# Kernel optimization log

Hardware: AMD Instinct MI355X
Metric: run time of the kernel (lower is better)

## Reference

```python
import jax, jax.numpy as jnp
import numpy as np

B, S, IK, IV = 16, 2048, 3, 1
D = IK + IV          # input_size = 4
H = 256              # hidden_size
F = 512              # dim_feedforward
L = 2                # num_layers
EPS = 1e-5


def setup_inputs() -> dict:
    key = jax.random.key(0)
    ks = jax.random.split(key, 16)
    n = jax.random.normal
    inp = {
        'KEY': n(ks[0], (B, S, IK), jnp.float32),
        'VALUE': n(ks[1], (B, S, IV), jnp.float32),
        # per-layer kernel-attention projections (stacked on layer axis)
        'Wq': n(ks[2], (L, D, H), jnp.float32) * 0.1,
        'bq': jnp.zeros((L, H), jnp.float32),
        'Wk': n(ks[3], (L, D, H), jnp.float32) * 0.1,
        'bk': jnp.zeros((L, H), jnp.float32),
        'Wv': n(ks[4], (L, D, H), jnp.float32) * 0.1,
        'bv': jnp.zeros((L, H), jnp.float32),
        'Wo': n(ks[5], (L, H, D), jnp.float32) * 0.1,
        'bo': jnp.zeros((L, D), jnp.float32),
        'bw': jnp.ones((L,), jnp.float32),          # Gaussian kernel bandwidth
        # LayerNorm 1
        'g1': jnp.ones((L, D), jnp.float32),
        'be1': jnp.zeros((L, D), jnp.float32),
        # FFN
        'W1': n(ks[6], (L, D, F), jnp.float32) * 0.1,
        'b1': jnp.zeros((L, F), jnp.float32),
        'W2': n(ks[7], (L, F, D), jnp.float32) * 0.1,
        'b2': jnp.zeros((L, D), jnp.float32),
        # LayerNorm 2
        'g2': jnp.ones((L, D), jnp.float32),
        'be2': jnp.zeros((L, D), jnp.float32),
        # final fc: input_size -> input_v
        'Wfc': n(ks[8], (D, IV), jnp.float32) * 0.1,
        'bfc': jnp.zeros((IV,), jnp.float32),
    }
    return inp


def _layernorm(x, g, b):
    m = x.mean(-1, keepdims=True)
    v = ((x - m) ** 2).mean(-1, keepdims=True)
    return (x - m) * jax.lax.rsqrt(v + EPS) * g + b


def reference(KEY, VALUE, Wq, bq, Wk, bk, Wv, bv, Wo, bo, bw,
              g1, be1, W1, b1, W2, b2, g2, be2, Wfc, bfc):
    # positioning: concat coords and values -> [B, S, D]
    X = jnp.concatenate([KEY, VALUE], axis=-1)
    n_layers = Wq.shape[0]
    for i in range(n_layers):
        # Nadaraya-Watson Gaussian kernel attention (madsnn, type='nwd', kernel='gauss')
        Q = X @ Wq[i] + bq[i]                      # [B,S,H]
        K = X @ Wk[i] + bk[i]                      # [B,S,H]
        V = X @ Wv[i] + bv[i]                      # [B,S,H]
        # pairwise squared distances ||q-k||^2, [B,S,S]
        d2 = ((Q * Q).sum(-1)[:, :, None]
              + (K * K).sum(-1)[:, None, :]
              - 2.0 * jnp.einsum('bqh,bkh->bqk', Q, K))
        attn = jax.nn.softmax(-0.5 * d2 * (bw[i] ** 2), axis=-1)
        attn_out = jnp.einsum('bqk,bkh->bqh', attn, V) @ Wo[i] + bo[i]  # [B,S,D]
        # residual + LayerNorm + FFN + residual + LayerNorm (dropout = identity in eval)
        res = _layernorm(X + attn_out, g1[i], be1[i])
        ff = jax.nn.relu(res @ W1[i] + b1[i]) @ W2[i] + b2[i]
        X = _layernorm(res + ff, g2[i], be2[i])
    return X @ Wfc + bfc                            # [B,S,IV]
```

## Files before the change

kernel.cpp:

```cpp
#include <hip/hip_runtime.h>

#define BB 16
#define SS 2048
#define NTOK (BB*SS)
#define FF 512
#define EPSF 1e-5f

#if __has_builtin(__builtin_amdgcn_exp2f)
#define EXP2F(x) __builtin_amdgcn_exp2f(x)
#else
#define EXP2F(x) exp2f(x)
#endif

typedef float v2f __attribute__((ext_vector_type(2)));


__device__ __forceinline__ float wred64(float v) {
#pragma unroll
  for (int m = 32; m > 0; m >>= 1) v += __shfl_xor(v, m, 64);
  return v;
}


__global__ __launch_bounds__(64) void prep_kernel(
    const float* __restrict__ Wq, const float* __restrict__ bq,
    const float* __restrict__ Wk, const float* __restrict__ bk,
    const float* __restrict__ Wv, const float* __restrict__ bv,
    const float* __restrict__ Wo, const float* __restrict__ bw,
    const float* __restrict__ W1, const float* __restrict__ b1,
    const float* __restrict__ W2,
    float* __restrict__ sm, float* __restrict__ w1t)
{
  const int i = blockIdx.x;
  const int lane = threadIdx.x;
  float m4[4][4] = {{0}}, gkk[4][4] = {{0}}, wvo[4][4] = {{0}};
  float akk[4] = {0}, bvo[4] = {0};
  float ck1 = 0.f, ck2 = 0.f;

  for (int h = lane; h < 256; h += 64) {
    float vq[4], vk[4], vv[4], wo4[4];
#pragma unroll
    for (int a = 0; a < 4; ++a) {
      vq[a]  = Wq[(i*4 + a)*256 + h];
      vk[a]  = Wk[(i*4 + a)*256 + h];
      vv[a]  = Wv[(i*4 + a)*256 + h];
      wo4[a] = Wo[(i*256 + h)*4 + a];
    }
    const float bqh = bq[i*256 + h], bkh = bk[i*256 + h], bvh = bv[i*256 + h];
#pragma unroll
    for (int a = 0; a < 4; ++a) {
#pragma unroll
      for (int c = 0; c < 4; ++c) {
        m4[a][c]  = fmaf(vq[a], vk[c], m4[a][c]);
        gkk[a][c] = fmaf(vk[a], vk[c], gkk[a][c]);
        wvo[a][c] = fmaf(vv[a], wo4[c], wvo[a][c]);
      }
      akk[a] = fmaf(vk[a], bqh - bkh, akk[a]);
      bvo[a] = fmaf(bvh, wo4[a], bvo[a]);
    }
    ck1 = fmaf(bqh, bkh, ck1);
    ck2 = fmaf(bkh, bkh, ck2);
  }
#pragma unroll
  for (int a = 0; a < 4; ++a) {
#pragma unroll
    for (int c = 0; c < 4; ++c) {
      m4[a][c]  = wred64(m4[a][c]);
      gkk[a][c] = wred64(gkk[a][c]);
      wvo[a][c] = wred64(wvo[a][c]);
    }
    akk[a] = wred64(akk[a]);
    bvo[a] = wred64(bvo[a]);
  }
  ck1 = wred64(ck1); ck2 = wred64(ck2);

  if (lane == 0) {
    const float bwv = bw[i];
    const float bw2 = bwv * bwv * 1.44269504088896f;
    float* s = sm + i*64;
#pragma unroll
    for (int a = 0; a < 4; ++a) {
#pragma unroll
      for (int c = 0; c < 4; ++c) {
        s[a*4+c]      = bw2 * m4[a][c];
        s[16 + a*4+c] = -0.5f * bw2 * gkk[a][c];
        s[32 + a*4+c] = wvo[a][c];
      }
      s[48+a] = bw2 * akk[a];
      s[52+a] = bvo[a];
    }
    s[56] = bw2 * (ck1 - 0.5f * ck2);
  }
  for (int f = lane; f < FF; f += 64) {
    float* rec = w1t + (i*FF + f)*12;
#pragma unroll
    for (int c = 0; c < 4; ++c) rec[c]   = W1[(i*4 + c)*FF + f];
#pragma unroll
    for (int c = 0; c < 4; ++c) rec[4+c] = W2[(i*FF + f)*4 + c];
    rec[8] = b1[i*FF + f];
    rec[9] = 0.f; rec[10] = 0.f; rec[11] = 0.f;
  }
}

__device__ __forceinline__ void compute_feat(const float x[4], const float* __restrict__ s,
                                             float* __restrict__ featrec)
{
  float P[4], VT[4], tk[4];
#pragma unroll
  for (int a = 0; a < 4; ++a) {
    P[a]  = fmaf(s[a*4+3], x[3], fmaf(s[a*4+2], x[2], fmaf(s[a*4+1], x[1], s[a*4+0]*x[0])));
    tk[a] = fmaf(s[16+a*4+3], x[3], fmaf(s[16+a*4+2], x[2], fmaf(s[16+a*4+1], x[1], s[16+a*4+0]*x[0])));
    VT[a] = s[52+a] + fmaf(s[32+3*4+a], x[3], fmaf(s[32+2*4+a], x[2], fmaf(s[32+1*4+a], x[1], s[32+0*4+a]*x[0])));
  }
  float R = s[56];
#pragma unroll
  for (int a = 0; a < 4; ++a) R = fmaf(tk[a] + s[48+a], x[a], R);
  float4* fp = (float4*)featrec;
  fp[0] = make_float4(P[0], P[1], P[2], P[3]);
  fp[1] = make_float4(VT[0], VT[1], VT[2], VT[3]);
  fp[2] = make_float4(R, 0.f, 0.f, 0.f);
}

__global__ __launch_bounds__(256) void feat_kernel(
    const float* __restrict__ KEY, const float* __restrict__ VALUE,
    const float* __restrict__ sm, float* __restrict__ feat)
{
  const int gq = blockIdx.x*256 + threadIdx.x;
  float xr[4] = {KEY[gq*3], KEY[gq*3+1], KEY[gq*3+2], VALUE[gq]};
  float fr[12];
  compute_feat(xr, sm, fr);
  float4* fp = (float4*)(feat + (size_t)gq*12);
  fp[0] = ((float4*)fr)[0];
  fp[1] = ((float4*)fr)[1];
  fp[2] = ((float4*)fr)[2];
}

__device__ __forceinline__ void ln4(const float t[4], const float* __restrict__ g,
                                    const float* __restrict__ b, float r[4])
{
  const float m = 0.25f*(t[0]+t[1]+t[2]+t[3]);
  const float d0 = t[0]-m, d1 = t[1]-m, d2 = t[2]-m, d3 = t[3]-m;
  const float v = 0.25f*(d0*d0 + d1*d1 + d2*d2 + d3*d3);
  const float sc = rsqrtf(v + EPSF);
  r[0] = fmaf(d0*sc, g[0], b[0]);
  r[1] = fmaf(d1*sc, g[1], b[1]);
  r[2] = fmaf(d2*sc, g[2], b[2]);
  r[3] = fmaf(d3*sc, g[3], b[3]);
}

__global__ __launch_bounds__(1024, 4) void layer_kernel(
    const float* __restrict__ KEY, const float* __restrict__ VALUE,
    const float* __restrict__ X, const float* __restrict__ feat,
    const float* __restrict__ w1t, const float* __restrict__ smn,
    const float* __restrict__ bo, const float* __restrict__ g1, const float* __restrict__ be1,
    const float* __restrict__ b2v, const float* __restrict__ g2, const float* __restrict__ be2,
    float* __restrict__ Xout, float* __restrict__ featout,
    const float* __restrict__ Wfc, const float* __restrict__ bfc,
    float* __restrict__ outp, int first, int last)
{
  const int bid = blockIdx.x;
  const int b = bid >> 4, qg = bid & 15;
  const int qbase = (b << 11) + (qg << 7);
  const int kbase = b << 11;
  const int tid = threadIdx.x;
  const int lane = tid & 63;
  const int wv = __builtin_amdgcn_readfirstlane(tid >> 6);

  __shared__ float smem[12288 + 512];
  float* red  = smem;
  float* ress = smem + 12288;
  float* redf = smem;

  v2f xq0, xq1, xq2, xq3;
  if (first) {
    const int qa = qbase + lane, qb = qa + 64;
    xq0 = v2f{KEY[qa*3    ], KEY[qb*3    ]};
    xq1 = v2f{KEY[qa*3 + 1], KEY[qb*3 + 1]};
    xq2 = v2f{KEY[qa*3 + 2], KEY[qb*3 + 2]};
    xq3 = v2f{VALUE[qa], VALUE[qb]};
  } else {
    const float4 xa = *(const float4*)(X + (size_t)(qbase + lane     )*4);
    const float4 xb = *(const float4*)(X + (size_t)(qbase + 64 + lane)*4);
    xq0 = v2f{xa.x, xb.x}; xq1 = v2f{xa.y, xb.y};
    xq2 = v2f{xa.z, xb.z}; xq3 = v2f{xa.w, xb.w};
  }

  v2f aaxy = v2f{0.f,0.f}, aazw = v2f{0.f,0.f};
  v2f abxy = v2f{0.f,0.f}, abzw = v2f{0.f,0.f};
  v2f ad   = v2f{0.f,0.f};

  const float* kf = feat + (size_t)(kbase + (wv << 7)) * 12;
#pragma unroll 4
  for (int k = 0; k < 128; ++k) {
    const float4 P  = *(const float4*)(kf + k*12);
    const float4 VT = *(const float4*)(kf + k*12 + 4);
    const float  R  = kf[k*12 + 8];
    v2f l = xq0 * v2f{P.x, P.x};
    l = __builtin_elementwise_fma(xq1, v2f{P.y, P.y}, l);
    l = __builtin_elementwise_fma(xq2, v2f{P.z, P.z}, l);
    l = __builtin_elementwise_fma(xq3, v2f{P.w, P.w}, l);
    const float e0 = EXP2F(l.x + R);
    const float e1 = EXP2F(l.y + R);
    const v2f Vxy = v2f{VT.x, VT.y}, Vzw = v2f{VT.z, VT.w};
    const v2f e0v = v2f{e0, e0}, e1v = v2f{e1, e1};
    aaxy = __builtin_elementwise_fma(e0v, Vxy, aaxy);
    aazw = __builtin_elementwise_fma(e0v, Vzw, aazw);
    abxy = __builtin_elementwise_fma(e1v, Vxy, abxy);
    abzw = __builtin_elementwise_fma(e1v, Vzw, abzw);
    ad += v2f{e0, e1};
  }

  {
    float* rr = red + (size_t)((wv << 6) + lane)*12;
    *(float4*)rr       = make_float4(aaxy.x, aaxy.y, aazw.x, aazw.y);
    *(float4*)(rr + 4) = make_float4(abxy.x, abxy.y, abzw.x, abzw.y);
    rr[8] = ad.x; rr[9] = ad.y;
  }
  __syncthreads();

  if (tid < 128) {
    const int ql = tid & 63, sel = tid >> 6;
    float s0 = 0.f, s1 = 0.f, s2 = 0.f, s3 = 0.f, sd = 0.f;
#pragma unroll
    for (int w = 0; w < 16; ++w) {
      const float* rr = red + (size_t)((w << 6) + ql)*12;
      const float4 vv = *(const float4*)(rr + sel*4);
      s0 += vv.x; s1 += vv.y; s2 += vv.z; s3 += vv.w;
      sd += rr[8 + sel];
    }
    const float inv = 1.0f / sd;
    const int gq = qbase + tid;
    float xv0, xv1, xv2, xv3;
    if (first) {
      xv0 = KEY[gq*3]; xv1 = KEY[gq*3+1]; xv2 = KEY[gq*3+2]; xv3 = VALUE[gq];
    } else {
      const float4 xv = *(const float4*)(X + (size_t)gq*4);
      xv0 = xv.x; xv1 = xv.y; xv2 = xv.z; xv3 = xv.w;
    }
    float t4[4];
    t4[0] = xv0 + fmaf(s0, inv, bo[0]);
    t4[1] = xv1 + fmaf(s1, inv, bo[1]);
    t4[2] = xv2 + fmaf(s2, inv, bo[2]);
    t4[3] = xv3 + fmaf(s3, inv, bo[3]);
    float r[4];
    ln4(t4, g1, be1, r);
    *(float4*)(ress + tid*4) = make_float4(r[0], r[1], r[2], r[3]);
  }
  __syncthreads();

  const int tok = tid & 127, fc = tid >> 7;
  const float4 rv = *(const float4*)(ress + tok*4);
  float fa0 = 0.f, fa1 = 0.f, fa2 = 0.f, fa3 = 0.f;
  const float* wt = w1t + (size_t)fc*64*12;
#pragma unroll 4
  for (int f = 0; f < 64; ++f) {
    const float* rec = wt + f*12;
    const float4 w1r = *(const float4*)rec;
    const float4 w2r = *(const float4*)(rec + 4);
    const float b1f = rec[8];
    float h = fmaf(rv.w, w1r.w, fmaf(rv.z, w1r.z, fmaf(rv.y, w1r.y, fmaf(rv.x, w1r.x, b1f))));
    h = fmaxf(h, 0.f);
    fa0 = fmaf(h, w2r.x, fa0);
    fa1 = fmaf(h, w2r.y, fa1);
    fa2 = fmaf(h, w2r.z, fa2);
    fa3 = fmaf(h, w2r.w, fa3);
  }
  *(float4*)(redf + (size_t)((fc << 7) + tok)*4) = make_float4(fa0, fa1, fa2, fa3);
  __syncthreads();

  if (tid < 128) {
    float t2[4];
#pragma unroll
    for (int c = 0; c < 4; ++c) {
      float s = b2v[c];
#pragma unroll
      for (int k = 0; k < 8; ++k) s += redf[(size_t)((k << 7) + tid)*4 + c];
      t2[c] = ress[tid*4 + c] + s;
    }
    float y[4];
    ln4(t2, g2, be2, y);
    const int gq = qbase + tid;
    if (last) {
      outp[gq] = fmaf(y[3], Wfc[3], fmaf(y[2], Wfc[2], fmaf(y[1], Wfc[1], fmaf(y[0], Wfc[0], bfc[0]))));
    } else {
      *(float4*)(Xout + (size_t)gq*4) = make_float4(y[0], y[1], y[2], y[3]);
      float fr[12];
      compute_feat(y, smn, fr);
      float4* fp = (float4*)(featout + (size_t)gq*12);
      fp[0] = ((float4*)fr)[0];
      fp[1] = ((float4*)fr)[1];
      fp[2] = ((float4*)fr)[2];
    }
  }
}

extern "C" void kernel_launch(void* const* d_in, const int* in_sizes, int n_in,
                              void* d_out, int out_size, void* d_ws, size_t ws_size,
                              hipStream_t stream)
{
  const float* KEY   = (const float*)d_in[0];
  const float* VALUE = (const float*)d_in[1];
  const float* Wq  = (const float*)d_in[2];
  const float* bq  = (const float*)d_in[3];
  const float* Wk  = (const float*)d_in[4];
  const float* bk  = (const float*)d_in[5];
  const float* Wv  = (const float*)d_in[6];
  const float* bv  = (const float*)d_in[7];
  const float* Wo  = (const float*)d_in[8];
  const float* bo  = (const float*)d_in[9];
  const float* bw  = (const float*)d_in[10];
  const float* g1  = (const float*)d_in[11];
  const float* be1 = (const float*)d_in[12];
  const float* W1  = (const float*)d_in[13];
  const float* b1  = (const float*)d_in[14];
  const float* W2  = (const float*)d_in[15];
  const float* b2  = (const float*)d_in[16];
  const float* g2  = (const float*)d_in[17];
  const float* be2 = (const float*)d_in[18];
  const float* Wfc = (const float*)d_in[19];
  const float* bfc = (const float*)d_in[20];
  float* out = (float*)d_out;

  float* w    = (float*)d_ws;
  float* sm   = w;
  float* w1t  = w + 128;
  float* X1   = w + 12416;
  float* f0   = w + 143488;
  float* f1   = w + 536704;

  prep_kernel<<<2, 64, 0, stream>>>(Wq, bq, Wk, bk, Wv, bv, Wo, bw,
                                    W1, b1, W2, sm, w1t);
  feat_kernel<<<128, 256, 0, stream>>>(KEY, VALUE, sm, f0);

  layer_kernel<<<256, 1024, 0, stream>>>(KEY, VALUE, X1, f0,
      w1t, sm + 64,
      bo, g1, be1, b2, g2, be2,
      X1, f1, Wfc, bfc, out, 1, 0);

  layer_kernel<<<256, 1024, 0, stream>>>(KEY, VALUE, X1, f1,
      w1t + FF*12, sm,
      bo + 4, g1 + 4, be1 + 4, b2 + 4, g2 + 4, be2 + 4,
      X1, f1, Wfc, bfc, out, 0, 1);
}
```

Baseline: 183.9 us.

## Restructure kernel attention: wave-uniform query tiles over planar paired key features

Key features are stored in a planar structure-of-arrays layout that packs two tokens per float4, and the per-token record shrinks from 12 to 9 floats. In the attention loop each wave now holds 8 queries in wave-uniform (scalar) registers, and each lane streams coalesced key pairs. Partial sums are combined with wave shuffle reductions instead of a large shared-memory reduction. Blocks shrink to 512 threads covering 64 queries, with twice as many blocks. The aim is to reuse each key load across more queries and to cut LDS traffic. The cost is scattered scalar stores when writing the next layer's features and 40 shuffle reductions per wave.

```diff
diff --git a/kernel.cpp b/kernel.cpp
--- a/kernel.cpp
+++ b/kernel.cpp
@@ -3,6 +3,8 @@
 #define BB 16
 #define SS 2048
 #define NTOK (BB*SS)
+#define NPAIR (NTOK/2)
+#define PLANE (NPAIR*4)
 #define FF 512
 #define EPSF 1e-5f
 
@@ -19,6 +21,12 @@
 #pragma unroll
   for (int m = 32; m > 0; m >>= 1) v += __shfl_xor(v, m, 64);
   return v;
+}
+
+__device__ __forceinline__ float rflf(float v) {
+  union { float f; int i; } u; u.f = v;
+  u.i = __builtin_amdgcn_readfirstlane(u.i);
+  return u.f;
 }
 
 
@@ -115,24 +123,29 @@
   float R = s[56];
 #pragma unroll
   for (int a = 0; a < 4; ++a) R = fmaf(tk[a] + s[48+a], x[a], R);
-  float4* fp = (float4*)featrec;
-  fp[0] = make_float4(P[0], P[1], P[2], P[3]);
-  fp[1] = make_float4(VT[0], VT[1], VT[2], VT[3]);
-  fp[2] = make_float4(R, 0.f, 0.f, 0.f);
+  featrec[0]=P[0]; featrec[1]=P[1]; featrec[2]=P[2]; featrec[3]=P[3];
+  featrec[4]=VT[0]; featrec[5]=VT[1]; featrec[6]=VT[2]; featrec[7]=VT[3];
+  featrec[8]=R;
 }
 
 __global__ __launch_bounds__(256) void feat_kernel(
     const float* __restrict__ KEY, const float* __restrict__ VALUE,
     const float* __restrict__ sm, float* __restrict__ feat)
 {
-  const int gq = blockIdx.x*256 + threadIdx.x;
-  float xr[4] = {KEY[gq*3], KEY[gq*3+1], KEY[gq*3+2], VALUE[gq]};
-  float fr[12];
-  compute_feat(xr, sm, fr);
-  float4* fp = (float4*)(feat + (size_t)gq*12);
-  fp[0] = ((float4*)fr)[0];
-  fp[1] = ((float4*)fr)[1];
-  fp[2] = ((float4*)fr)[2];
+  const int p = blockIdx.x*256 + threadIdx.x;
+  const int ta = 2*p, tb = 2*p + 1;
+  float xa[4] = {KEY[ta*3], KEY[ta*3+1], KEY[ta*3+2], VALUE[ta]};
+  float xb[4] = {KEY[tb*3], KEY[tb*3+1], KEY[tb*3+2], VALUE[tb]};
+  float fa[9], fb[9];
+  compute_feat(xa, sm, fa);
+  compute_feat(xb, sm, fb);
+#pragma unroll
+  for (int pl = 0; pl < 4; ++pl) {
+    *(float4*)(feat + (size_t)pl*PLANE + (size_t)p*4) =
+        make_float4(fa[2*pl], fb[2*pl], fa[2*pl+1], fb[2*pl+1]);
+  }
+  *(float4*)(feat + (size_t)4*PLANE + (size_t)p*4) =
+      make_float4(fa[8], fb[8], 0.f, 0.f);
 }
 
 __device__ __forceinline__ void ln4(const float t[4], const float* __restrict__ g,
@@ -148,7 +161,7 @@
   r[3] = fmaf(d3*sc, g[3], b[3]);
 }
 
-__global__ __launch_bounds__(1024, 4) void layer_kernel(
+__global__ __launch_bounds__(512, 4) void layer_kernel(
     const float* __restrict__ KEY, const float* __restrict__ VALUE,
     const float* __restrict__ X, const float* __restrict__ feat,
     const float* __restrict__ w1t, const float* __restrict__ smn,
@@ -159,76 +172,94 @@
     float* __restrict__ outp, int first, int last)
 {
   const int bid = blockIdx.x;
-  const int b = bid >> 4, qg = bid & 15;
-  const int qbase = (b << 11) + (qg << 7);
-  const int kbase = b << 11;
+  const int b = bid >> 5, qg = bid & 31;
+  const int qbase = (b << 11) + (qg << 6);
   const int tid = threadIdx.x;
-  const int lane = tid & 63;
-  const int wv = __builtin_amdgcn_readfirstlane(tid >> 6);
-
-  __shared__ float smem[12288 + 512];
-  float* red  = smem;
-  float* ress = smem + 12288;
-  float* redf = smem;
-
-  v2f xq0, xq1, xq2, xq3;
-  if (first) {
-    const int qa = qbase + lane, qb = qa + 64;
-    xq0 = v2f{KEY[qa*3    ], KEY[qb*3    ]};
-    xq1 = v2f{KEY[qa*3 + 1], KEY[qb*3 + 1]};
-    xq2 = v2f{KEY[qa*3 + 2], KEY[qb*3 + 2]};
-    xq3 = v2f{VALUE[qa], VALUE[qb]};
-  } else {
-    const float4 xa = *(const float4*)(X + (size_t)(qbase + lane     )*4);
-    const float4 xb = *(const float4*)(X + (size_t)(qbase + 64 + lane)*4);
-    xq0 = v2f{xa.x, xb.x}; xq1 = v2f{xa.y, xb.y};
-    xq2 = v2f{xa.z, xb.z}; xq3 = v2f{xa.w, xb.w};
-  }
-
-  v2f aaxy = v2f{0.f,0.f}, aazw = v2f{0.f,0.f};
-  v2f abxy = v2f{0.f,0.f}, abzw = v2f{0.f,0.f};
-  v2f ad   = v2f{0.f,0.f};
-
-  const float* kf = feat + (size_t)(kbase + (wv << 7)) * 12;
-#pragma unroll 4
-  for (int k = 0; k < 128; ++k) {
-    const float4 P  = *(const float4*)(kf + k*12);
-    const float4 VT = *(const float4*)(kf + k*12 + 4);
-    const float  R  = kf[k*12 + 8];
-    v2f l = xq0 * v2f{P.x, P.x};
-    l = __builtin_elementwise_fma(xq1, v2f{P.y, P.y}, l);
-    l = __builtin_elementwise_fma(xq2, v2f{P.z, P.z}, l);
-    l = __builtin_elementwise_fma(xq3, v2f{P.w, P.w}, l);
-    const float e0 = EXP2F(l.x + R);
-    const float e1 = EXP2F(l.y + R);
-    const v2f Vxy = v2f{VT.x, VT.y}, Vzw = v2f{VT.z, VT.w};
-    const v2f e0v = v2f{e0, e0}, e1v = v2f{e1, e1};
-    aaxy = __builtin_elementwise_fma(e0v, Vxy, aaxy);
-    aazw = __builtin_elementwise_fma(e0v, Vzw, aazw);
-    abxy = __builtin_elementwise_fma(e1v, Vxy, abxy);
-    abzw = __builtin_elementwise_fma(e1v, Vzw, abzw);
-    ad += v2f{e0, e1};
-  }
-
-  {
-    float* rr = red + (size_t)((wv << 6) + lane)*12;
-    *(float4*)rr       = make_float4(aaxy.x, aaxy.y, aazw.x, aazw.y);
-    *(float4*)(rr + 4) = make_float4(abxy.x, abxy.y, abzw.x, abzw.y);
-    rr[8] = ad.x; rr[9] = ad.y;
+  const int lane = tid & 63, wv = tid >> 6;
+  const int q0 = qbase + wv*8;
+
+  __shared__ float sums[8*8*9];
+  __shared__ float ress[64*4];
+  __shared__ float redf[8*64*4];
+
+  float qx0[8], qx1[8], qx2[8], qx3[8];
+#pragma unroll
+  for (int q = 0; q < 8; ++q) {
+    const int gq = q0 + q;
+    float a, bq_, c, d;
+    if (first) {
+      a = KEY[gq*3]; bq_ = KEY[gq*3+1]; c = KEY[gq*3+2]; d = VALUE[gq];
+    } else {
+      const float4 xv = *(const float4*)(X + (size_t)gq*4);
+      a = xv.x; bq_ = xv.y; c = xv.z; d = xv.w;
+    }
+    qx0[q] = rflf(a); qx1[q] = rflf(bq_); qx2[q] = rflf(c); qx3[q] = rflf(d);
+  }
+
+  v2f aV0[8], aV1[8], aV2[8], aV3[8], aD[8];
+#pragma unroll
+  for (int q = 0; q < 8; ++q) {
+    aV0[q] = v2f{0.f,0.f}; aV1[q] = v2f{0.f,0.f};
+    aV2[q] = v2f{0.f,0.f}; aV3[q] = v2f{0.f,0.f};
+    aD[q]  = v2f{0.f,0.f};
+  }
+
+  const int pb = (b << 10) + lane;
+#pragma unroll 2
+  for (int it = 0; it < 16; ++it) {
+    const size_t p4 = (size_t)(pb + (it << 6)) * 4;
+    const float4 A = *(const float4*)(feat + p4);
+    const float4 Bf = *(const float4*)(feat + (size_t)PLANE + p4);
+    const float4 C = *(const float4*)(feat + (size_t)2*PLANE + p4);
+    const float4 D = *(const float4*)(feat + (size_t)3*PLANE + p4);
+    const float4 E = *(const float4*)(feat + (size_t)4*PLANE + p4);
+    const v2f P0 = v2f{A.x, A.y},  P1 = v2f{A.z, A.w};
+    const v2f P2 = v2f{Bf.x, Bf.y}, P3 = v2f{Bf.z, Bf.w};
+    const v2f V0 = v2f{C.x, C.y},  V1 = v2f{C.z, C.w};
+    const v2f V2 = v2f{D.x, D.y},  V3 = v2f{D.z, D.w};
+    const v2f Rp = v2f{E.x, E.y};
+#pragma unroll
+    for (int q = 0; q < 8; ++q) {
+      v2f l = __builtin_elementwise_fma(P0, v2f{qx0[q], qx0[q]}, Rp);
+      l = __builtin_elementwise_fma(P1, v2f{qx1[q], qx1[q]}, l);
+      l = __builtin_elementwise_fma(P2, v2f{qx2[q], qx2[q]}, l);
+      l = __builtin_elementwise_fma(P3, v2f{qx3[q], qx3[q]}, l);
+      const v2f e = v2f{EXP2F(l.x), EXP2F(l.y)};
+      aV0[q] = __builtin_elementwise_fma(e, V0, aV0[q]);
+      aV1[q] = __builtin_elementwise_fma(e, V1, aV1[q]);
+      aV2[q] = __builtin_elementwise_fma(e, V2, aV2[q]);
+      aV3[q] = __builtin_elementwise_fma(e, V3, aV3[q]);
+      aD[q] += e;
+    }
+  }
+
+  float s[8][5];
+#pragma unroll
+  for (int q = 0; q < 8; ++q) {
+    s[q][0] = aV0[q].x + aV0[q].y;
+    s[q][1] = aV1[q].x + aV1[q].y;
+    s[q][2] = aV2[q].x + aV2[q].y;
+    s[q][3] = aV3[q].x + aV3[q].y;
+    s[q][4] = aD[q].x + aD[q].y;
+  }
+#pragma unroll
+  for (int q = 0; q < 8; ++q)
+#pragma unroll
+    for (int c = 0; c < 5; ++c) s[q][c] = wred64(s[q][c]);
+
+  if (lane == 0) {
+    float* dst = sums + wv*72;
+#pragma unroll
+    for (int q = 0; q < 8; ++q) {
+#pragma unroll
+      for (int c = 0; c < 5; ++c) dst[q*9 + c] = s[q][c];
+    }
   }
   __syncthreads();
 
-  if (tid < 128) {
-    const int ql = tid & 63, sel = tid >> 6;
-    float s0 = 0.f, s1 = 0.f, s2 = 0.f, s3 = 0.f, sd = 0.f;
-#pragma unroll
-    for (int w = 0; w < 16; ++w) {
-      const float* rr = red + (size_t)((w << 6) + ql)*12;
-      const float4 vv = *(const float4*)(rr + sel*4);
-      s0 += vv.x; s1 += vv.y; s2 += vv.z; s3 += vv.w;
-      sd += rr[8 + sel];
-    }
-    const float inv = 1.0f / sd;
+  if (tid < 64) {
+    const float* sv = sums + tid*9;
+    const float inv = 1.0f / sv[4];
     const int gq = qbase + tid;
     float xv0, xv1, xv2, xv3;
     if (first) {
@@ -238,17 +269,17 @@
       xv0 = xv.x; xv1 = xv.y; xv2 = xv.z; xv3 = xv.w;
     }
     float t4[4];
-    t4[0] = xv0 + fmaf(s0, inv, bo[0]);
-    t4[1] = xv1 + fmaf(s1, inv, bo[1]);
-    t4[2] = xv2 + fmaf(s2, inv, bo[2]);
-    t4[3] = xv3 + fmaf(s3, inv, bo[3]);
+    t4[0] = xv0 + fmaf(sv[0], inv, bo[0]);
+    t4[1] = xv1 + fmaf(sv[1], inv, bo[1]);
+    t4[2] = xv2 + fmaf(sv[2], inv, bo[2]);
+    t4[3] = xv3 + fmaf(sv[3], inv, bo[3]);
     float r[4];
     ln4(t4, g1, be1, r);
     *(float4*)(ress + tid*4) = make_float4(r[0], r[1], r[2], r[3]);
   }
   __syncthreads();
 
-  const int tok = tid & 127, fc = tid >> 7;
+  const int tok = lane, fc = wv;
   const float4 rv = *(const float4*)(ress + tok*4);
   float fa0 = 0.f, fa1 = 0.f, fa2 = 0.f, fa3 = 0.f;
   const float* wt = w1t + (size_t)fc*64*12;
@@ -265,17 +296,17 @@
     fa2 = fmaf(h, w2r.z, fa2);
     fa3 = fmaf(h, w2r.w, fa3);
   }
-  *(float4*)(redf + (size_t)((fc << 7) + tok)*4) = make_float4(fa0, fa1, fa2, fa3);
+  *(float4*)(redf + (size_t)((fc << 6) + tok)*4) = make_float4(fa0, fa1, fa2, fa3);
   __syncthreads();
 
-  if (tid < 128) {
+  if (tid < 64) {
     float t2[4];
 #pragma unroll
     for (int c = 0; c < 4; ++c) {
-      float s = b2v[c];
-#pragma unroll
-      for (int k = 0; k < 8; ++k) s += redf[(size_t)((k << 7) + tid)*4 + c];
-      t2[c] = ress[tid*4 + c] + s;
+      float sa = b2v[c];
+#pragma unroll
+      for (int k = 0; k < 8; ++k) sa += redf[(size_t)((k << 6) + tid)*4 + c];
+      t2[c] = ress[tid*4 + c] + sa;
     }
     float y[4];
     ln4(t2, g2, be2, y);
@@ -284,12 +315,13 @@
       outp[gq] = fmaf(y[3], Wfc[3], fmaf(y[2], Wfc[2], fmaf(y[1], Wfc[1], fmaf(y[0], Wfc[0], bfc[0]))));
     } else {
       *(float4*)(Xout + (size_t)gq*4) = make_float4(y[0], y[1], y[2], y[3]);
-      float fr[12];
+      float fr[9];
       compute_feat(y, smn, fr);
-      float4* fp = (float4*)(featout + (size_t)gq*12);
-      fp[0] = ((float4*)fr)[0];
-      fp[1] = ((float4*)fr)[1];
-      fp[2] = ((float4*)fr)[2];
+      const int p = gq >> 1, par = gq & 1;
+#pragma unroll
+      for (int c = 0; c < 8; ++c)
+        featout[(size_t)(c >> 1)*PLANE + (size_t)p*4 + (c & 1)*2 + par] = fr[c];
+      featout[(size_t)4*PLANE + (size_t)p*4 + par] = fr[8];
     }
   }
 }
@@ -326,18 +358,18 @@
   float* w1t  = w + 128;
   float* X1   = w + 12416;
   float* f0   = w + 143488;
-  float* f1   = w + 536704;
+  float* f1   = w + 471168;
 
   prep_kernel<<<2, 64, 0, stream>>>(Wq, bq, Wk, bk, Wv, bv, Wo, bw,
                                     W1, b1, W2, sm, w1t);
-  feat_kernel<<<128, 256, 0, stream>>>(KEY, VALUE, sm, f0);
-
-  layer_kernel<<<256, 1024, 0, stream>>>(KEY, VALUE, X1, f0,
+  feat_kernel<<<64, 256, 0, stream>>>(KEY, VALUE, sm, f0);
+
+  layer_kernel<<<512, 512, 0, stream>>>(KEY, VALUE, X1, f0,
       w1t, sm + 64,
       bo, g1, be1, b2, g2, be2,
       X1, f1, Wfc, bfc, out, 1, 0);
 
-  layer_kernel<<<256, 1024, 0, stream>>>(KEY, VALUE, X1, f1,
+  layer_kernel<<<512, 512, 0, stream>>>(KEY, VALUE, X1, f1,
       w1t + FF*12, sm,
       bo + 4, g1 + 4, be1 + 4, b2 + 4, g2 + 4, be2 + 4,
       X1, f1, Wfc, bfc, out, 0, 1);
```

Measured after the change: 183.1 us. About the same (-0.4%).
